# Kernel tuning notes

Measured on AMD Instinct MI355X. Metric: run time of the kernel, lower is better.

The kernel has to match this reference:

```python
import jax, jax.numpy as jnp
import numpy as np

B, S, C = 2, 4096, 512
H = 8            # num heads
D = C // H       # head dim = 64


def setup_inputs() -> dict:
    key = jax.random.key(0)
    ks = jax.random.split(key, 5)
    s = 0.02
    return {
        "hidden_states": jax.random.normal(ks[0], (B, S, C), dtype=jnp.float32),
        "Wq": jax.random.normal(ks[1], (C, C), dtype=jnp.float32) * s,
        "Wk": jax.random.normal(ks[2], (C, C), dtype=jnp.float32) * s,
        "Wv": jax.random.normal(ks[3], (C, C), dtype=jnp.float32) * s,
        "Wo": jax.random.normal(ks[4], (C, C), dtype=jnp.float32) * s,
        "bo": jnp.zeros((C,), dtype=jnp.float32),
    }


def reference(hidden_states, Wq, Wk, Wv, Wo, bo):
    # Self-attention path of AttnProcessor (encoder_hidden_states=None,
    # no norms, no mask, residual_connection=False, rescale=1.0).
    b, s, c = hidden_states.shape
    scale = jnp.float32(D) ** -0.5
    # QKV projections (Linear, no bias as in diffusers defaults)
    q = hidden_states @ Wq.T   # [b,s,c]
    k = hidden_states @ Wk.T
    v = hidden_states @ Wv.T
    # head_to_batch_dim: [b,s,c] -> [b,s,h,d]
    q = q.reshape(b, s, H, D)
    k = k.reshape(b, s, H, D)
    v = v.reshape(b, s, H, D)
    # get_attention_scores: scaled QK^T + softmax (full O(S^2) matrix, as in source)
    scores = jnp.einsum("bqhd,bkhd->bhqk", q, k) * scale   # [b,h,s,s]
    probs = jax.nn.softmax(scores, axis=-1)
    # bmm with V, batch_to_head_dim
    out = jnp.einsum("bhqk,bkhd->bqhd", probs, v).reshape(b, s, c)
    # to_out[0] (Linear with bias); to_out[1] is Dropout (identity at eval)
    out = out @ Wo.T + bo
    return out
```

## Files before the change

### kernel.cpp

```cpp
#include <hip/hip_runtime.h>
#include <hip/hip_bf16.h>

#define BB 2
#define SS 4096
#define CC 512
#define HH 8
#define DD 64
#define MM (BB*SS)

typedef __bf16 bf16;
typedef __attribute__((ext_vector_type(8))) __bf16 bf16x8;
typedef __attribute__((ext_vector_type(4))) __bf16 bf16x4;
typedef __attribute__((ext_vector_type(4))) float f32x4;

#define LP 72
#define QSCALE 0.18033688f

__device__ __forceinline__ float exp2_fast(float x) {
  float r;
  asm("v_exp_f32 %0, %1" : "=v"(r) : "v"(x));
  return r;
}

__device__ __forceinline__ bf16x8 cvt8(const float4 a, const float4 b) {
  bf16x8 r;
  r[0]=(bf16)a.x; r[1]=(bf16)a.y; r[2]=(bf16)a.z; r[3]=(bf16)a.w;
  r[4]=(bf16)b.x; r[5]=(bf16)b.y; r[6]=(bf16)b.z; r[7]=(bf16)b.w;
  return r;
}

__global__ __launch_bounds__(256) void cvt_f32_bf16(
    const float* __restrict__ src, bf16* __restrict__ dst)
{
  size_t e = ((size_t)blockIdx.x * 256 + threadIdx.x) * 8;
  float4 a = ((const float4*)(src + e))[0];
  float4 b = ((const float4*)(src + e))[1];
  *(bf16x8*)(dst + e) = cvt8(a, b);
}

__global__ __launch_bounds__(256) void qkv_gemm(
    const bf16* __restrict__ Xb,
    const float* __restrict__ Wq, const float* __restrict__ Wk,
    const float* __restrict__ Wv,
    bf16* __restrict__ qp, bf16* __restrict__ kp, bf16* __restrict__ vtp)
{
  __shared__ bf16 Aa[64*LP];
  __shared__ bf16 Ab[64*LP];
  __shared__ bf16 Bt[64*LP];
  const int m0 = blockIdx.x * 128;
  const int nf = blockIdx.y * 64;
  const int tens = nf >> 9;
  const int n0 = nf & 511;
  const float* W = (tens == 0) ? Wq : ((tens == 1) ? Wk : Wv);

  const int t = threadIdx.x;
  const int w = t >> 6;
  const int lane = t & 63;
  const int l15 = lane & 15;
  const int quad = lane >> 4;
  const int srow = t >> 2;
  const int scol = (t & 3) << 4;

  f32x4 aca[4], acb[4];
  #pragma unroll
  for (int i = 0; i < 4; ++i)
    #pragma unroll
    for (int j = 0; j < 4; ++j) { aca[i][j] = 0.f; acb[i][j] = 0.f; }

  for (int k0 = 0; k0 < CC; k0 += 64) {
    __syncthreads();
    {
      const bf16* sa = Xb + (size_t)(m0 + srow) * CC + k0 + scol;
      *(bf16x8*)&Aa[srow*LP + scol]     = ((const bf16x8*)sa)[0];
      *(bf16x8*)&Aa[srow*LP + scol + 8] = ((const bf16x8*)sa)[1];
      const bf16* sb = Xb + (size_t)(m0 + 64 + srow) * CC + k0 + scol;
      *(bf16x8*)&Ab[srow*LP + scol]     = ((const bf16x8*)sb)[0];
      *(bf16x8*)&Ab[srow*LP + scol + 8] = ((const bf16x8*)sb)[1];
      const float* s1 = W + (size_t)(n0 + srow) * CC + k0 + scol;
      float4 b0 = ((const float4*)s1)[0];
      float4 b1 = ((const float4*)s1)[1];
      float4 b2 = ((const float4*)s1)[2];
      float4 b3 = ((const float4*)s1)[3];
      *(bf16x8*)&Bt[srow*LP + scol]     = cvt8(b0, b1);
      *(bf16x8*)&Bt[srow*LP + scol + 8] = cvt8(b2, b3);
    }
    __syncthreads();
    #pragma unroll
    for (int c = 0; c < 2; ++c) {
      bf16x8 afa = *(const bf16x8*)&Aa[(w*16 + l15)*LP + c*32 + quad*8];
      bf16x8 afb = *(const bf16x8*)&Ab[(w*16 + l15)*LP + c*32 + quad*8];
      #pragma unroll
      for (int nt = 0; nt < 4; ++nt) {
        bf16x8 bfr = *(const bf16x8*)&Bt[(nt*16 + l15)*LP + c*32 + quad*8];
        aca[nt] = __builtin_amdgcn_mfma_f32_16x16x32_bf16(afa, bfr, aca[nt], 0, 0, 0);
        acb[nt] = __builtin_amdgcn_mfma_f32_16x16x32_bf16(afb, bfr, acb[nt], 0, 0, 0);
      }
    }
  }

  if (tens == 0) {
    #pragma unroll
    for (int nt = 0; nt < 4; ++nt)
      #pragma unroll
      for (int r = 0; r < 4; ++r) { aca[nt][r] *= QSCALE; acb[nt][r] *= QSCALE; }
  }

  const int h = n0 >> 6;
  bf16* plane = (tens == 0) ? qp : ((tens == 1) ? kp : vtp);
  const int c8 = (t & 7) * 8;

  {
    const int mt0 = m0;
    const int b = mt0 >> 12, s0g = mt0 & 4095;
    __syncthreads();
    if (tens < 2) {
      #pragma unroll
      for (int nt = 0; nt < 4; ++nt)
        #pragma unroll
        for (int r = 0; r < 4; ++r)
          Aa[(w*16 + quad*4 + r)*LP + nt*16 + l15] = (bf16)aca[nt][r];
    } else {
      #pragma unroll
      for (int nt = 0; nt < 4; ++nt)
        #pragma unroll
        for (int r = 0; r < 4; ++r)
          Aa[(nt*16 + l15)*LP + w*16 + quad*4 + r] = (bf16)aca[nt][r];
    }
    __syncthreads();
    #pragma unroll
    for (int i = 0; i < 2; ++i) {
      const int row = (t >> 3) + 32*i;
      bf16x8 v = *(const bf16x8*)&Aa[row*LP + c8];
      if (tens < 2) {
        *(bf16x8*)&plane[((size_t)((b*HH + h)*SS) + s0g + row)*DD + c8] = v;
      } else {
        *(bf16x8*)&plane[((size_t)((b*HH + h)*DD) + row)*SS + s0g + c8] = v;
      }
    }
  }

  {
    const int mt0 = m0 + 64;
    const int b = mt0 >> 12, s0g = mt0 & 4095;
    __syncthreads();
    if (tens < 2) {
      #pragma unroll
      for (int nt = 0; nt < 4; ++nt)
        #pragma unroll
        for (int r = 0; r < 4; ++r)
          Aa[(w*16 + quad*4 + r)*LP + nt*16 + l15] = (bf16)acb[nt][r];
    } else {
      #pragma unroll
      for (int nt = 0; nt < 4; ++nt)
        #pragma unroll
        for (int r = 0; r < 4; ++r)
          Aa[(nt*16 + l15)*LP + w*16 + quad*4 + r] = (bf16)acb[nt][r];
    }
    __syncthreads();
    #pragma unroll
    for (int i = 0; i < 2; ++i) {
      const int row = (t >> 3) + 32*i;
      bf16x8 v = *(const bf16x8*)&Aa[row*LP + c8];
      if (tens < 2) {
        *(bf16x8*)&plane[((size_t)((b*HH + h)*SS) + s0g + row)*DD + c8] = v;
      } else {
        *(bf16x8*)&plane[((size_t)((b*HH + h)*DD) + row)*SS + s0g + c8] = v;
      }
    }
  }
}

__global__ __launch_bounds__(256) void attn_fa(
    const bf16* __restrict__ qpl, const bf16* __restrict__ kpl,
    const bf16* __restrict__ vtpl, bf16* __restrict__ aout)
{
  __shared__ bf16 Kt[2][64*LP];
  __shared__ bf16 Vt[2][64*LP];

  const int t = threadIdx.x;
  const int w = t >> 6;
  const int lane = t & 63;
  const int l15 = lane & 15;
  const int quad = lane >> 4;

  const int bh = blockIdx.y;
  const int q0 = blockIdx.x * 128;
  const size_t plane = (size_t)SS * DD;
  const bf16* Qp = qpl + (size_t)bh * plane;
  const bf16* Kp = kpl + (size_t)bh * plane;
  const bf16* Vg = vtpl + (size_t)bh * plane;

  bf16x8 qf[2][2];
  #pragma unroll
  for (int wq = 0; wq < 2; ++wq) {
    const bf16* qr = Qp + (size_t)(q0 + w*32 + wq*16 + l15) * DD + quad*8;
    qf[wq][0] = *(const bf16x8*)qr;
    qf[wq][1] = *(const bf16x8*)(qr + 32);
  }

  f32x4 o[2][4];
  float rs[2] = {0.f, 0.f};
  #pragma unroll
  for (int wq = 0; wq < 2; ++wq)
    #pragma unroll
    for (int nt = 0; nt < 4; ++nt)
      #pragma unroll
      for (int r = 0; r < 4; ++r) o[wq][nt][r] = 0.f;

  const int r0 = t >> 3;
  const int c0 = (t & 7) * 8;
  const int koff = (c0 >> 5)*32 + ((c0 >> 3) & 3)*4;

  bf16x8 ka0, ka1;
  bf16x4 v00, v01, v10, v11;
  {
    ka0 = *(const bf16x8*)&Kp[(size_t)r0*DD + c0];
    ka1 = *(const bf16x8*)&Kp[(size_t)(r0 + 32)*DD + c0];
    v00 = *(const bf16x4*)&Vg[(size_t)r0*SS + koff];
    v01 = *(const bf16x4*)&Vg[(size_t)r0*SS + koff + 16];
    v10 = *(const bf16x4*)&Vg[(size_t)(r0+32)*SS + koff];
    v11 = *(const bf16x4*)&Vg[(size_t)(r0+32)*SS + koff + 16];
    *(bf16x8*)&Kt[0][r0*LP + c0]      = ka0;
    *(bf16x8*)&Kt[0][(r0+32)*LP + c0] = ka1;
    bf16x8 vv;
    vv[0]=v00[0]; vv[1]=v00[1]; vv[2]=v00[2]; vv[3]=v00[3];
    vv[4]=v01[0]; vv[5]=v01[1]; vv[6]=v01[2]; vv[7]=v01[3];
    *(bf16x8*)&Vt[0][r0*LP + c0] = vv;
    vv[0]=v10[0]; vv[1]=v10[1]; vv[2]=v10[2]; vv[3]=v10[3];
    vv[4]=v11[0]; vv[5]=v11[1]; vv[6]=v11[2]; vv[7]=v11[3];
    *(bf16x8*)&Vt[0][(r0+32)*LP + c0] = vv;
  }
  __syncthreads();

  for (int it = 0; it < SS/64; ++it) {
    const int cur = it & 1;
    if (it < SS/64 - 1) {
      const int kb = (it + 1) * 64;
      ka0 = *(const bf16x8*)&Kp[(size_t)(kb + r0)*DD + c0];
      ka1 = *(const bf16x8*)&Kp[(size_t)(kb + r0 + 32)*DD + c0];
      v00 = *(const bf16x4*)&Vg[(size_t)r0*SS + kb + koff];
      v01 = *(const bf16x4*)&Vg[(size_t)r0*SS + kb + koff + 16];
      v10 = *(const bf16x4*)&Vg[(size_t)(r0+32)*SS + kb + koff];
      v11 = *(const bf16x4*)&Vg[(size_t)(r0+32)*SS + kb + koff + 16];
    }

    f32x4 st[2][4];
    #pragma unroll
    for (int nt = 0; nt < 4; ++nt) {
      bf16x8 kf0 = *(const bf16x8*)&Kt[cur][(nt*16 + l15)*LP + quad*8];
      bf16x8 kf1 = *(const bf16x8*)&Kt[cur][(nt*16 + l15)*LP + 32 + quad*8];
      #pragma unroll
      for (int wq = 0; wq < 2; ++wq) {
        f32x4 z; z[0]=z[1]=z[2]=z[3]=0.f;
        z = __builtin_amdgcn_mfma_f32_16x16x32_bf16(kf0, qf[wq][0], z, 0, 0, 0);
        z = __builtin_amdgcn_mfma_f32_16x16x32_bf16(kf1, qf[wq][1], z, 0, 0, 0);
        st[wq][nt] = z;
      }
    }

    bf16x8 pb[2][2];
    #pragma unroll
    for (int wq = 0; wq < 2; ++wq) {
      float acc_s = 0.f;
      #pragma unroll
      for (int nt = 0; nt < 4; ++nt)
        #pragma unroll
        for (int r = 0; r < 4; ++r) {
          float pv = exp2_fast(st[wq][nt][r]);
          acc_s += pv;
          pb[wq][nt >> 1][(nt & 1)*4 + r] = (bf16)pv;
        }
      rs[wq] += acc_s;
    }

    #pragma unroll
    for (int kbh = 0; kbh < 2; ++kbh) {
      #pragma unroll
      for (int nt = 0; nt < 4; ++nt) {
        bf16x8 vf = *(const bf16x8*)&Vt[cur][(nt*16 + l15)*LP + kbh*32 + quad*8];
        #pragma unroll
        for (int wq = 0; wq < 2; ++wq)
          o[wq][nt] = __builtin_amdgcn_mfma_f32_16x16x32_bf16(vf, pb[wq][kbh], o[wq][nt], 0, 0, 0);
      }
    }

    if (it < SS/64 - 1) {
      const int nxt = cur ^ 1;
      *(bf16x8*)&Kt[nxt][r0*LP + c0]      = ka0;
      *(bf16x8*)&Kt[nxt][(r0+32)*LP + c0] = ka1;
      bf16x8 vv;
      vv[0]=v00[0]; vv[1]=v00[1]; vv[2]=v00[2]; vv[3]=v00[3];
      vv[4]=v01[0]; vv[5]=v01[1]; vv[6]=v01[2]; vv[7]=v01[3];
      *(bf16x8*)&Vt[nxt][r0*LP + c0] = vv;
      vv[0]=v10[0]; vv[1]=v10[1]; vv[2]=v10[2]; vv[3]=v10[3];
      vv[4]=v11[0]; vv[5]=v11[1]; vv[6]=v11[2]; vv[7]=v11[3];
      *(bf16x8*)&Vt[nxt][(r0+32)*LP + c0] = vv;
      __syncthreads();
    }
  }

  const int b = bh >> 3, h = bh & 7;
  #pragma unroll
  for (int wq = 0; wq < 2; ++wq) {
    float s = rs[wq];
    s += __shfl_xor(s, 16);
    s += __shfl_xor(s, 32);
    const float inv = 1.f / s;
    const size_t row = (size_t)(b*SS + q0 + w*32 + wq*16 + l15) * CC + h*DD;
    #pragma unroll
    for (int nt = 0; nt < 4; ++nt) {
      bf16x4 ov;
      #pragma unroll
      for (int r = 0; r < 4; ++r) ov[r] = (bf16)(o[wq][nt][r] * inv);
      *(bf16x4*)&aout[row + nt*16 + quad*4] = ov;
    }
  }
}

__global__ __launch_bounds__(256) void out_gemm(
    const bf16* __restrict__ A, const bf16* __restrict__ Wob,
    const float* __restrict__ bo, float* __restrict__ out)
{
  __shared__ bf16 Aa[64*LP];
  __shared__ bf16 Ab[64*LP];
  __shared__ bf16 Bt[64*LP];
  const int m0 = blockIdx.x * 128;
  const int n0 = blockIdx.y * 64;

  const int t = threadIdx.x;
  const int w = t >> 6;
  const int lane = t & 63;
  const int l15 = lane & 15;
  const int quad = lane >> 4;
  const int srow = t >> 2;
  const int scol = (t & 3) << 4;

  f32x4 aca[4], acb[4];
  #pragma unroll
  for (int i = 0; i < 4; ++i)
    #pragma unroll
    for (int j = 0; j < 4; ++j) { aca[i][j] = 0.f; acb[i][j] = 0.f; }

  for (int k0 = 0; k0 < CC; k0 += 64) {
    __syncthreads();
    {
      const bf16* sa = A + (size_t)(m0 + srow) * CC + k0 + scol;
      *(bf16x8*)&Aa[srow*LP + scol]     = ((const bf16x8*)sa)[0];
      *(bf16x8*)&Aa[srow*LP + scol + 8] = ((const bf16x8*)sa)[1];
      const bf16* sb = A + (size_t)(m0 + 64 + srow) * CC + k0 + scol;
      *(bf16x8*)&Ab[srow*LP + scol]     = ((const bf16x8*)sb)[0];
      *(bf16x8*)&Ab[srow*LP + scol + 8] = ((const bf16x8*)sb)[1];
      const bf16* s1 = Wob + (size_t)(n0 + srow) * CC + k0 + scol;
      *(bf16x8*)&Bt[srow*LP + scol]     = ((const bf16x8*)s1)[0];
      *(bf16x8*)&Bt[srow*LP + scol + 8] = ((const bf16x8*)s1)[1];
    }
    __syncthreads();
    #pragma unroll
    for (int c = 0; c < 2; ++c) {
      bf16x8 afa = *(const bf16x8*)&Aa[(w*16 + l15)*LP + c*32 + quad*8];
      bf16x8 afb = *(const bf16x8*)&Ab[(w*16 + l15)*LP + c*32 + quad*8];
      #pragma unroll
      for (int nt = 0; nt < 4; ++nt) {
        bf16x8 bfr = *(const bf16x8*)&Bt[(nt*16 + l15)*LP + c*32 + quad*8];
        aca[nt] = __builtin_amdgcn_mfma_f32_16x16x32_bf16(afa, bfr, aca[nt], 0, 0, 0);
        acb[nt] = __builtin_amdgcn_mfma_f32_16x16x32_bf16(afb, bfr, acb[nt], 0, 0, 0);
      }
    }
  }

  #pragma unroll
  for (int nt = 0; nt < 4; ++nt) {
    const int ng = n0 + nt*16 + l15;
    const float bias = bo[ng];
    #pragma unroll
    for (int r = 0; r < 4; ++r) {
      const int mga = m0 + w*16 + quad*4 + r;
      out[(size_t)mga*CC + ng] = aca[nt][r] + bias;
      const int mgb = m0 + 64 + w*16 + quad*4 + r;
      out[(size_t)mgb*CC + ng] = acb[nt][r] + bias;
    }
  }
}

extern "C" void kernel_launch(void* const* d_in, const int* in_sizes, int n_in,
                              void* d_out, int out_size, void* d_ws, size_t ws_size,
                              hipStream_t stream) {
  const float* hs = (const float*)d_in[0];
  const float* Wq = (const float*)d_in[1];
  const float* Wk = (const float*)d_in[2];
  const float* Wv = (const float*)d_in[3];
  const float* Wo = (const float*)d_in[4];
  const float* bo = (const float*)d_in[5];
  float* out = (float*)d_out;

  const size_t PE = (size_t)BB*HH*SS*DD;
  bf16* ws   = (bf16*)d_ws;
  bf16* qp   = ws;
  bf16* kp   = ws + PE;
  bf16* vtp  = ws + 2*PE;
  bf16* Xb   = ws + 3*PE;
  bf16* aout = ws + 3*PE;
  bf16* Wob  = qp;

  cvt_f32_bf16<<<dim3(2048),      256, 0, stream>>>(hs, Xb);
  qkv_gemm<<<dim3(MM/128, 24),    256, 0, stream>>>(Xb, Wq, Wk, Wv, qp, kp, vtp);
  attn_fa <<<dim3(SS/128, BB*HH), 256, 0, stream>>>(qp, kp, vtp, aout);
  cvt_f32_bf16<<<dim3(128),       256, 0, stream>>>(Wo, Wob);
  out_gemm<<<dim3(MM/128, CC/64), 256, 0, stream>>>(aout, Wob, bo, out);
}
```

Before: 204.5 us.

## Pre-convert QKV weights to bf16 and widen QKV GEMM tile to 128x128

Adds a separate kernel that converts Wq/Wk/Wv to bf16 once, folding the softmax scale into Wq, so the QKV GEMM no longer re-reads and converts fp32 weights in every block. The QKV GEMM tile grows from 128x64 to 128x128, which halves the grid and doubles the MFMA work done per loaded A fragment. The cost is an extra launch, extra workspace, and twice as many accumulator registers, which may lower occupancy. Scaling the weights before rounding to bf16 changes rounding slightly compared with scaling the outputs.

```diff
diff --git a/kernel.cpp b/kernel.cpp
--- a/kernel.cpp
+++ b/kernel.cpp
@@ -38,20 +38,34 @@
   *(bf16x8*)(dst + e) = cvt8(a, b);
 }
 
+__global__ __launch_bounds__(256) void cvt_w(
+    const float* __restrict__ Wq, const float* __restrict__ Wk,
+    const float* __restrict__ Wv, bf16* __restrict__ Wb)
+{
+  size_t e = ((size_t)blockIdx.x * 256 + threadIdx.x) * 8;
+  const int tens = (int)(e >> 18);
+  const float* src = ((tens == 0) ? Wq : (tens == 1) ? Wk : Wv) + (e & 262143);
+  const float sc = (tens == 0) ? QSCALE : 1.f;
+  float4 a = ((const float4*)src)[0];
+  float4 b = ((const float4*)src)[1];
+  bf16x8 r;
+  r[0]=(bf16)(a.x*sc); r[1]=(bf16)(a.y*sc); r[2]=(bf16)(a.z*sc); r[3]=(bf16)(a.w*sc);
+  r[4]=(bf16)(b.x*sc); r[5]=(bf16)(b.y*sc); r[6]=(bf16)(b.z*sc); r[7]=(bf16)(b.w*sc);
+  *(bf16x8*)(Wb + e) = r;
+}
+
 __global__ __launch_bounds__(256) void qkv_gemm(
-    const bf16* __restrict__ Xb,
-    const float* __restrict__ Wq, const float* __restrict__ Wk,
-    const float* __restrict__ Wv,
+    const bf16* __restrict__ Xb, const bf16* __restrict__ Wb,
     bf16* __restrict__ qp, bf16* __restrict__ kp, bf16* __restrict__ vtp)
 {
   __shared__ bf16 Aa[64*LP];
   __shared__ bf16 Ab[64*LP];
-  __shared__ bf16 Bt[64*LP];
-  const int m0 = blockIdx.x * 128;
-  const int nf = blockIdx.y * 64;
-  const int tens = nf >> 9;
-  const int n0 = nf & 511;
-  const float* W = (tens == 0) ? Wq : ((tens == 1) ? Wk : Wv);
+  __shared__ bf16 Ba[64*LP];
+  __shared__ bf16 Bb[64*LP];
+  const int m0  = blockIdx.x * 128;
+  const int nf0 = blockIdx.y * 128;
+  const int tens = nf0 >> 9;
+  const int n0 = nf0 & 511;
 
   const int t = threadIdx.x;
   const int w = t >> 6;
@@ -61,11 +75,15 @@
   const int srow = t >> 2;
   const int scol = (t & 3) << 4;
 
-  f32x4 aca[4], acb[4];
-  #pragma unroll
-  for (int i = 0; i < 4; ++i)
-    #pragma unroll
-    for (int j = 0; j < 4; ++j) { aca[i][j] = 0.f; acb[i][j] = 0.f; }
+  f32x4 acc[2][2][4];
+  #pragma unroll
+  for (int mi = 0; mi < 2; ++mi)
+    #pragma unroll
+    for (int ni = 0; ni < 2; ++ni)
+      #pragma unroll
+      for (int nt = 0; nt < 4; ++nt)
+        #pragma unroll
+        for (int r = 0; r < 4; ++r) acc[mi][ni][nt][r] = 0.f;
 
   for (int k0 = 0; k0 < CC; k0 += 64) {
     __syncthreads();
@@ -76,13 +94,12 @@
       const bf16* sb = Xb + (size_t)(m0 + 64 + srow) * CC + k0 + scol;
       *(bf16x8*)&Ab[srow*LP + scol]     = ((const bf16x8*)sb)[0];
       *(bf16x8*)&Ab[srow*LP + scol + 8] = ((const bf16x8*)sb)[1];
-      const float* s1 = W + (size_t)(n0 + srow) * CC + k0 + scol;
-      float4 b0 = ((const float4*)s1)[0];
-      float4 b1 = ((const float4*)s1)[1];
-      float4 b2 = ((const float4*)s1)[2];
-      float4 b3 = ((const float4*)s1)[3];
-      *(bf16x8*)&Bt[srow*LP + scol]     = cvt8(b0, b1);
-      *(bf16x8*)&Bt[srow*LP + scol + 8] = cvt8(b2, b3);
+      const bf16* s1 = Wb + (size_t)(nf0 + srow) * CC + k0 + scol;
+      *(bf16x8*)&Ba[srow*LP + scol]     = ((const bf16x8*)s1)[0];
+      *(bf16x8*)&Ba[srow*LP + scol + 8] = ((const bf16x8*)s1)[1];
+      const bf16* s2 = Wb + (size_t)(nf0 + 64 + srow) * CC + k0 + scol;
+      *(bf16x8*)&Bb[srow*LP + scol]     = ((const bf16x8*)s2)[0];
+      *(bf16x8*)&Bb[srow*LP + scol + 8] = ((const bf16x8*)s2)[1];
     }
     __syncthreads();
     #pragma unroll
@@ -91,40 +108,35 @@
       bf16x8 afb = *(const bf16x8*)&Ab[(w*16 + l15)*LP + c*32 + quad*8];
       #pragma unroll
       for (int nt = 0; nt < 4; ++nt) {
-        bf16x8 bfr = *(const bf16x8*)&Bt[(nt*16 + l15)*LP + c*32 + quad*8];
-        aca[nt] = __builtin_amdgcn_mfma_f32_16x16x32_bf16(afa, bfr, aca[nt], 0, 0, 0);
-        acb[nt] = __builtin_amdgcn_mfma_f32_16x16x32_bf16(afb, bfr, acb[nt], 0, 0, 0);
-      }
-    }
-  }
-
-  if (tens == 0) {
-    #pragma unroll
-    for (int nt = 0; nt < 4; ++nt)
-      #pragma unroll
-      for (int r = 0; r < 4; ++r) { aca[nt][r] *= QSCALE; acb[nt][r] *= QSCALE; }
-  }
-
-  const int h = n0 >> 6;
+        bf16x8 ba = *(const bf16x8*)&Ba[(nt*16 + l15)*LP + c*32 + quad*8];
+        bf16x8 bb = *(const bf16x8*)&Bb[(nt*16 + l15)*LP + c*32 + quad*8];
+        acc[0][0][nt] = __builtin_amdgcn_mfma_f32_16x16x32_bf16(afa, ba, acc[0][0][nt], 0, 0, 0);
+        acc[1][0][nt] = __builtin_amdgcn_mfma_f32_16x16x32_bf16(afb, ba, acc[1][0][nt], 0, 0, 0);
+        acc[0][1][nt] = __builtin_amdgcn_mfma_f32_16x16x32_bf16(afa, bb, acc[0][1][nt], 0, 0, 0);
+        acc[1][1][nt] = __builtin_amdgcn_mfma_f32_16x16x32_bf16(afb, bb, acc[1][1][nt], 0, 0, 0);
+      }
+    }
+  }
+
   bf16* plane = (tens == 0) ? qp : ((tens == 1) ? kp : vtp);
   const int c8 = (t & 7) * 8;
 
-  {
-    const int mt0 = m0;
+  auto epi = [&](const f32x4* as, int mt0, int nb) {
     const int b = mt0 >> 12, s0g = mt0 & 4095;
+    const int h = nb >> 6;
     __syncthreads();
     if (tens < 2) {
       #pragma unroll
       for (int nt = 0; nt < 4; ++nt)
         #pragma unroll
         for (int r = 0; r < 4; ++r)
-          Aa[(w*16 + quad*4 + r)*LP + nt*16 + l15] = (bf16)aca[nt][r];
+          Aa[(w*16 + quad*4 + r)*LP + nt*16 + l15] = (bf16)as[nt][r];
     } else {
       #pragma unroll
       for (int nt = 0; nt < 4; ++nt)
         #pragma unroll
         for (int r = 0; r < 4; ++r)
-          Aa[(nt*16 + l15)*LP + w*16 + quad*4 + r] = (bf16)aca[nt][r];
+          Aa[(nt*16 + l15)*LP + w*16 + quad*4 + r] = (bf16)as[nt][r];
     }
     __syncthreads();
     #pragma unroll
@@ -137,37 +149,12 @@
         *(bf16x8*)&plane[((size_t)((b*HH + h)*DD) + row)*SS + s0g + c8] = v;
       }
     }
-  }
-
-  {
-    const int mt0 = m0 + 64;
-    const int b = mt0 >> 12, s0g = mt0 & 4095;
-    __syncthreads();
-    if (tens < 2) {
-      #pragma unroll
-      for (int nt = 0; nt < 4; ++nt)
-        #pragma unroll
-        for (int r = 0; r < 4; ++r)
-          Aa[(w*16 + quad*4 + r)*LP + nt*16 + l15] = (bf16)acb[nt][r];
-    } else {
-      #pragma unroll
-      for (int nt = 0; nt < 4; ++nt)
-        #pragma unroll
-        for (int r = 0; r < 4; ++r)
-          Aa[(nt*16 + l15)*LP + w*16 + quad*4 + r] = (bf16)acb[nt][r];
-    }
-    __syncthreads();
-    #pragma unroll
-    for (int i = 0; i < 2; ++i) {
-      const int row = (t >> 3) + 32*i;
-      bf16x8 v = *(const bf16x8*)&Aa[row*LP + c8];
-      if (tens < 2) {
-        *(bf16x8*)&plane[((size_t)((b*HH + h)*SS) + s0g + row)*DD + c8] = v;
-      } else {
-        *(bf16x8*)&plane[((size_t)((b*HH + h)*DD) + row)*SS + s0g + c8] = v;
-      }
-    }
-  }
+  };
+
+  epi(acc[0][0], m0,      n0);
+  epi(acc[1][0], m0 + 64, n0);
+  epi(acc[0][1], m0,      n0 + 64);
+  epi(acc[1][1], m0 + 64, n0 + 64);
 }
 
 __global__ __launch_bounds__(256) void attn_fa(
@@ -401,9 +388,11 @@
   bf16* Xb   = ws + 3*PE;
   bf16* aout = ws + 3*PE;
   bf16* Wob  = qp;
+  bf16* Wb   = ws + 4*PE;
 
   cvt_f32_bf16<<<dim3(2048),      256, 0, stream>>>(hs, Xb);
-  qkv_gemm<<<dim3(MM/128, 24),    256, 0, stream>>>(Xb, Wq, Wk, Wv, qp, kp, vtp);
+  cvt_w       <<<dim3(384),       256, 0, stream>>>(Wq, Wk, Wv, Wb);
+  qkv_gemm<<<dim3(MM/128, 12),    256, 0, stream>>>(Xb, Wb, qp, kp, vtp);
   attn_fa <<<dim3(SS/128, BB*HH), 256, 0, stream>>>(qp, kp, vtp, aout);
   cvt_f32_bf16<<<dim3(128),       256, 0, stream>>>(Wo, Wob);
   out_gemm<<<dim3(MM/128, CC/64), 256, 0, stream>>>(aout, Wob, bo, out);
```

Result: no change. 200.5 us (-2.0%).
